# Performance work log

Measured on AMD Instinct MI355X. Metric: run time of the kernel, lower is better.

## Reference

```python
import jax, jax.numpy as jnp
import numpy as np

N_NODES = 50000
N_GRAPHS = 64


def gcn_conv(x, W, b, src, dst, n_nodes):
    # PyG GCNConv: add self-loops, symmetric normalization D^-1/2 A D^-1/2,
    # linear transform, scatter-sum aggregation from src -> dst, plus bias.
    si = jnp.arange(n_nodes, dtype=src.dtype)
    s = jnp.concatenate([src, si])
    d = jnp.concatenate([dst, si])
    deg = jax.ops.segment_sum(jnp.ones_like(d, dtype=x.dtype), d, num_segments=n_nodes)
    dinv = jax.lax.rsqrt(jnp.maximum(deg, 1.0))  # deg >= 1 due to self-loops
    norm = dinv[s] * dinv[d]                      # [E+N]
    h = x @ W                                     # [N, out]
    msg = h[s] * norm[:, None]                    # gather + scale
    out = jax.ops.segment_sum(msg, d, num_segments=n_nodes)
    return out + b


def setup_inputs() -> dict:
    key = jax.random.key(0)
    ks = jax.random.split(key, 12)
    input_dim, hidden, half = 128, 64, 32
    x = jax.random.normal(ks[0], (N_NODES, input_dim), dtype=jnp.float32)
    edge_index = jax.random.randint(ks[1], (2, 800000), 0, N_NODES, dtype=jnp.int64)
    batch = jnp.sort(jax.random.randint(ks[2], (N_NODES,), 0, N_GRAPHS, dtype=jnp.int64))
    def lin(k, fan_in, fan_out):
        s = 1.0 / np.sqrt(fan_in)
        return jax.random.uniform(k, (fan_in, fan_out), jnp.float32, -s, s)
    return {
        "x": x,
        "edge_index": edge_index,
        "batch": batch,
        "W1": lin(ks[3], input_dim, hidden), "b1": jnp.zeros((hidden,), jnp.float32),
        "W2": lin(ks[4], hidden, hidden),    "b2": jnp.zeros((hidden,), jnp.float32),
        "Wc1": lin(ks[5], hidden, half),     "bc1": jnp.zeros((half,), jnp.float32),
        "Wc2": lin(ks[6], half, 1),          "bc2": jnp.zeros((1,), jnp.float32),
    }


def reference(x, edge_index, batch, W1, b1, W2, b2, Wc1, bc1, Wc2, bc2):
    src, dst = edge_index[0], edge_index[1]
    h = jax.nn.relu(gcn_conv(x, W1, b1, src, dst, N_NODES))
    # F.dropout(training=False) -> identity in eval
    h = jax.nn.relu(gcn_conv(h, W2, b2, src, dst, N_NODES))
    # global_mean_pool over graphs
    sums = jax.ops.segment_sum(h, batch, num_segments=N_GRAPHS)
    cnts = jax.ops.segment_sum(jnp.ones((h.shape[0], 1), h.dtype), batch, num_segments=N_GRAPHS)
    g = sums / jnp.maximum(cnts, 1.0)             # [G, hidden]
    # MLP head (Dropout(0.2) is identity in eval)
    z = jax.nn.relu(g @ Wc1 + bc1)
    return z @ Wc2 + bc2                          # [G, 1]
```

## Files before the change

kernel.cpp:

```cpp
#include <hip/hip_runtime.h>
#include <math.h>

#define NG 64
#define HID 64
#define ELL 64

typedef __attribute__((ext_vector_type(8))) short bf16x8;
typedef __attribute__((ext_vector_type(4))) float f32x4;

__device__ __forceinline__ unsigned int bfbits(float f) {
    unsigned int u = __float_as_uint(f);
    return (u + 0x7FFFu + ((u >> 16) & 1u)) >> 16;
}
__device__ __forceinline__ float bfval(unsigned int bits) {
    return __uint_as_float(bits << 16);
}

__global__ void k_zero(int4* __restrict__ p, int n4) {
    int i = blockIdx.x * blockDim.x + threadIdx.x;
    if (i < n4) p[i] = make_int4(0, 0, 0, 0);
}

__global__ void k_degfill(const int* __restrict__ src, const int* __restrict__ dst,
                          int E, int* __restrict__ deg, int* __restrict__ col_ell) {
    int e = blockIdx.x * blockDim.x + threadIdx.x;
    if (e >= E) return;
    int d = dst[e];
    int slot = atomicAdd(deg + d, 1);
    if (slot < ELL) col_ell[(size_t)d * ELL + slot] = src[e];
}

__global__ __launch_bounds__(256) void k_aux(const int* __restrict__ deg,
                                             const int* __restrict__ batch,
                                             float* __restrict__ dinv,
                                             int* __restrict__ gstart,
                                             const float* __restrict__ W1,
                                             const float* __restrict__ W2,
                                             unsigned short* __restrict__ W1hi,
                                             unsigned short* __restrict__ W1lo,
                                             unsigned short* __restrict__ W2hi,
                                             unsigned short* __restrict__ W2lo,
                                             int n, int nblk) {
    const int t = threadIdx.x;
    if (blockIdx.x >= nblk) {
        int idx = (blockIdx.x - nblk) * 256 + t;
        if (idx < 128 * 64) {
            int k = idx >> 6, c = idx & 63;
            float f = W1[idx];
            unsigned hb = bfbits(f);
            W1hi[c * 128 + k] = (unsigned short)hb;
            W1lo[c * 128 + k] = (unsigned short)bfbits(f - bfval(hb));
        } else if (idx < 128 * 64 + 64 * 64) {
            int i2 = idx - 128 * 64;
            int k = i2 >> 6, c = i2 & 63;
            float f = W2[i2];
            unsigned hb = bfbits(f);
            W2hi[c * 64 + k] = (unsigned short)hb;
            W2lo[c * 64 + k] = (unsigned short)bfbits(f - bfval(hb));
        }
        return;
    }
    int i = blockIdx.x * 256 + t;
    if (i < n) {
        dinv[i] = 1.0f / sqrtf((float)deg[i] + 1.0f);
        int bi = batch[i];
        int bp = (i == 0) ? -1 : batch[i - 1];
        for (int g = bp + 1; g <= bi; ++g) gstart[g] = i;
        if (i == n - 1)
            for (int g = bi + 1; g <= NG; ++g) gstart[g] = n;
    }
}

template<int K>
__global__ __launch_bounds__(256) void k_gemm_mfma(const float* __restrict__ A,
                                                   const unsigned short* __restrict__ Whi,
                                                   const unsigned short* __restrict__ Wlo,
                                                   const float* __restrict__ dinv,
                                                   float* __restrict__ out, int n) {
    const int wave = threadIdx.x >> 6, lane = threadIdx.x & 63;
    const int ntile2 = (n + 31) >> 5;
    const int tile2 = blockIdx.x * 4 + wave;
    if (tile2 >= ntile2) return;
    const int lrow = lane & 15;
    const int kgrp = lane >> 4;
    const int r0 = tile2 * 32 + lrow;
    const int r1 = r0 + 16;

    f32x4 acc0[4], acc1[4];
#pragma unroll
    for (int ct = 0; ct < 4; ++ct) {
        acc0[ct] = (f32x4){0.f, 0.f, 0.f, 0.f};
        acc1[ct] = (f32x4){0.f, 0.f, 0.f, 0.f};
    }

#pragma unroll
    for (int s = 0; s < K / 32; ++s) {
        float a0[8], a1[8];
        {
            const float* p0 = A + (size_t)r0 * K + s * 32 + kgrp * 8;
            const float* p1 = A + (size_t)r1 * K + s * 32 + kgrp * 8;
            float4 u0, u1, w0, w1;
            if (r0 < n) { u0 = *(const float4*)p0; u1 = *(const float4*)(p0 + 4); }
            else { u0 = make_float4(0.f,0.f,0.f,0.f); u1 = u0; }
            if (r1 < n) { w0 = *(const float4*)p1; w1 = *(const float4*)(p1 + 4); }
            else { w0 = make_float4(0.f,0.f,0.f,0.f); w1 = w0; }
            a0[0]=u0.x; a0[1]=u0.y; a0[2]=u0.z; a0[3]=u0.w;
            a0[4]=u1.x; a0[5]=u1.y; a0[6]=u1.z; a0[7]=u1.w;
            a1[0]=w0.x; a1[1]=w0.y; a1[2]=w0.z; a1[3]=w0.w;
            a1[4]=w1.x; a1[5]=w1.y; a1[6]=w1.z; a1[7]=w1.w;
        }
        bf16x8 ahi0, alo0, ahi1, alo1;
#pragma unroll
        for (int e = 0; e < 8; ++e) {
            unsigned hb0 = bfbits(a0[e]);
            ahi0[e] = (short)hb0;
            alo0[e] = (short)bfbits(a0[e] - bfval(hb0));
            unsigned hb1 = bfbits(a1[e]);
            ahi1[e] = (short)hb1;
            alo1[e] = (short)bfbits(a1[e] - bfval(hb1));
        }
#pragma unroll
        for (int ct = 0; ct < 4; ++ct) {
            const size_t wo = (size_t)(ct * 16 + lrow) * K + s * 32 + kgrp * 8;
            bf16x8 whi = *(const bf16x8*)(Whi + wo);
            bf16x8 wlo = *(const bf16x8*)(Wlo + wo);
            acc0[ct] = __builtin_amdgcn_mfma_f32_16x16x32_bf16(ahi0, whi, acc0[ct], 0, 0, 0);
            acc0[ct] = __builtin_amdgcn_mfma_f32_16x16x32_bf16(alo0, whi, acc0[ct], 0, 0, 0);
            acc0[ct] = __builtin_amdgcn_mfma_f32_16x16x32_bf16(ahi0, wlo, acc0[ct], 0, 0, 0);
            acc1[ct] = __builtin_amdgcn_mfma_f32_16x16x32_bf16(ahi1, whi, acc1[ct], 0, 0, 0);
            acc1[ct] = __builtin_amdgcn_mfma_f32_16x16x32_bf16(alo1, whi, acc1[ct], 0, 0, 0);
            acc1[ct] = __builtin_amdgcn_mfma_f32_16x16x32_bf16(ahi1, wlo, acc1[ct], 0, 0, 0);
        }
    }

#pragma unroll
    for (int r = 0; r < 4; ++r) {
        int o0 = tile2 * 32 + kgrp * 4 + r;
        if (o0 < n) {
            float dv = dinv[o0];
#pragma unroll
            for (int ct = 0; ct < 4; ++ct)
                out[(size_t)o0 * HID + ct * 16 + lrow] = acc0[ct][r] * dv;
        }
        int o1 = o0 + 16;
        if (o1 < n) {
            float dv = dinv[o1];
#pragma unroll
            for (int ct = 0; ct < 4; ++ct)
                out[(size_t)o1 * HID + ct * 16 + lrow] = acc1[ct][r] * dv;
        }
    }
}

__global__ __launch_bounds__(512) void k_gather_gemm2(const float* __restrict__ hs,
                                                      const int* __restrict__ deg,
                                                      const int* __restrict__ col_ell,
                                                      const float* __restrict__ dinv,
                                                      const float* __restrict__ bias,
                                                      const unsigned short* __restrict__ Whi,
                                                      const unsigned short* __restrict__ Wlo,
                                                      float* __restrict__ outB, int n) {
    __shared__ float Ash[32][68];
    const int wave = threadIdx.x >> 6, lane = threadIdx.x & 63;
    const int grp = lane >> 4, sub = lane & 15;
    const int row = wave * 4 + grp;
    const int node = blockIdx.x * 32 + row;
    const bool has = node < n;

    float4 acc = make_float4(0.f, 0.f, 0.f, 0.f);
    float di = 0.f;
    int j = 0, e = 0;
    const int* cbase = col_ell + (size_t)node * ELL;
    if (has) {
        e = min(deg[node], ELL);
        di = dinv[node];
        acc = *(const float4*)(hs + (size_t)node * HID + sub * 4);
    }
    while (__any(j < e)) {
        int cc[8];
#pragma unroll
        for (int t = 0; t < 8; ++t) cc[t] = (j + t < e) ? cbase[j + t] : -1;
        float4 vv[8];
#pragma unroll
        for (int t = 0; t < 8; ++t)
            if (cc[t] >= 0) vv[t] = *(const float4*)(hs + (size_t)cc[t] * HID + sub * 4);
#pragma unroll
        for (int t = 0; t < 8; ++t)
            if (cc[t] >= 0) {
                acc.x += vv[t].x; acc.y += vv[t].y;
                acc.z += vv[t].z; acc.w += vv[t].w;
            }
        j += 8;
    }
    {
        float4 bv = *(const float4*)(bias + sub * 4);
        float4 o;
        o.x = has ? fmaxf(fmaf(acc.x, di, bv.x), 0.f) : 0.f;
        o.y = has ? fmaxf(fmaf(acc.y, di, bv.y), 0.f) : 0.f;
        o.z = has ? fmaxf(fmaf(acc.z, di, bv.z), 0.f) : 0.f;
        o.w = has ? fmaxf(fmaf(acc.w, di, bv.w), 0.f) : 0.f;
        *(float4*)&Ash[row][sub * 4] = o;
    }
    __syncthreads();

    const int rt = wave >> 2, ct = wave & 3;
    const int lrow = lane & 15;
    const int kgrp = lane >> 4;
    f32x4 a = (f32x4){0.f, 0.f, 0.f, 0.f};
#pragma unroll
    for (int s = 0; s < 2; ++s) {
        const float* ap = &Ash[rt * 16 + lrow][s * 32 + kgrp * 8];
        float4 u0 = *(const float4*)ap;
        float4 u1 = *(const float4*)(ap + 4);
        float av[8] = {u0.x, u0.y, u0.z, u0.w, u1.x, u1.y, u1.z, u1.w};
        bf16x8 ahi, alo;
#pragma unroll
        for (int e2 = 0; e2 < 8; ++e2) {
            unsigned hb = bfbits(av[e2]);
            ahi[e2] = (short)hb;
            alo[e2] = (short)bfbits(av[e2] - bfval(hb));
        }
        const size_t wo = (size_t)(ct * 16 + lrow) * 64 + s * 32 + kgrp * 8;
        bf16x8 whi = *(const bf16x8*)(Whi + wo);
        bf16x8 wlo = *(const bf16x8*)(Wlo + wo);
        a = __builtin_amdgcn_mfma_f32_16x16x32_bf16(ahi, whi, a, 0, 0, 0);
        a = __builtin_amdgcn_mfma_f32_16x16x32_bf16(alo, whi, a, 0, 0, 0);
        a = __builtin_amdgcn_mfma_f32_16x16x32_bf16(ahi, wlo, a, 0, 0, 0);
    }
#pragma unroll
    for (int r = 0; r < 4; ++r) {
        int orow = blockIdx.x * 32 + rt * 16 + kgrp * 4 + r;
        if (orow < n)
            outB[(size_t)orow * HID + ct * 16 + lrow] = a[r] * dinv[orow];
    }
}

__global__ __launch_bounds__(256) void k_gather(const float* __restrict__ hs,
                                                const int* __restrict__ deg,
                                                const int* __restrict__ col_ell,
                                                const float* __restrict__ dinv,
                                                const float* __restrict__ bias,
                                                float* __restrict__ out, int n) {
    const int wave = threadIdx.x >> 6, lane = threadIdx.x & 63;
    const int grp = lane >> 4, sub = lane & 15;
    const int node = blockIdx.x * 16 + wave * 4 + grp;
    const bool has = node < n;

    float4 acc = make_float4(0.f, 0.f, 0.f, 0.f);
    float di = 0.f;
    int j = 0, e = 0;
    const int* cbase = col_ell + (size_t)node * ELL;
    if (has) {
        e = min(deg[node], ELL);
        di = dinv[node];
        acc = *(const float4*)(hs + (size_t)node * HID + sub * 4);
    }
    while (__any(j < e)) {
        int cc[8];
#pragma unroll
        for (int t = 0; t < 8; ++t) cc[t] = (j + t < e) ? cbase[j + t] : -1;
        float4 vv[8];
#pragma unroll
        for (int t = 0; t < 8; ++t)
            if (cc[t] >= 0) vv[t] = *(const float4*)(hs + (size_t)cc[t] * HID + sub * 4);
#pragma unroll
        for (int t = 0; t < 8; ++t)
            if (cc[t] >= 0) {
                acc.x += vv[t].x; acc.y += vv[t].y;
                acc.z += vv[t].z; acc.w += vv[t].w;
            }
        j += 8;
    }
    if (has) {
        float4 bv = *(const float4*)(bias + sub * 4);
        float4 o;
        o.x = fmaxf(fmaf(acc.x, di, bv.x), 0.f);
        o.y = fmaxf(fmaf(acc.y, di, bv.y), 0.f);
        o.z = fmaxf(fmaf(acc.z, di, bv.z), 0.f);
        o.w = fmaxf(fmaf(acc.w, di, bv.w), 0.f);
        *(float4*)(out + (size_t)node * HID + sub * 4) = o;
    }
}

__global__ __launch_bounds__(512) void k_poolhead(const float* __restrict__ h,
                                                  const int* __restrict__ gstart,
                                                  const float* __restrict__ Wc1,
                                                  const float* __restrict__ bc1,
                                                  const float* __restrict__ Wc2,
                                                  const float* __restrict__ bc2,
                                                  float* __restrict__ outp, int n) {
    const int g = blockIdx.x;
    const int lo = gstart[g], lo2 = gstart[g + 1];
    const int t = threadIdx.x;
    const int rg = t >> 4;
    const int c4 = (t & 15) * 4;
    float4 acc = make_float4(0.f, 0.f, 0.f, 0.f);
    for (int r = lo + rg; r < lo2; r += 32) {
        float4 v = *(const float4*)(h + (size_t)r * HID + c4);
        acc.x += v.x; acc.y += v.y; acc.z += v.z; acc.w += v.w;
    }
    __shared__ float4 red[32][16];
    __shared__ float gmv[HID];
    __shared__ float zs[32];
    red[rg][t & 15] = acc;
    __syncthreads();
    if (t < 16) {
        float4 s = red[0][t];
#pragma unroll
        for (int g2 = 1; g2 < 32; ++g2) {
            float4 v = red[g2][t];
            s.x += v.x; s.y += v.y; s.z += v.z; s.w += v.w;
        }
        float inv = 1.0f / fmaxf((float)(lo2 - lo), 1.0f);
        gmv[t * 4 + 0] = s.x * inv; gmv[t * 4 + 1] = s.y * inv;
        gmv[t * 4 + 2] = s.z * inv; gmv[t * 4 + 3] = s.w * inv;
    }
    __syncthreads();
    if (t < 32) {
        float z = bc1[t];
#pragma unroll 8
        for (int k = 0; k < HID; ++k) z = fmaf(gmv[k], Wc1[k * 32 + t], z);
        zs[t] = fmaxf(z, 0.f) * Wc2[t];
    }
    __syncthreads();
    if (t == 0) {
        float o = bc2[0];
#pragma unroll
        for (int j = 0; j < 32; ++j) o += zs[j];
        outp[g] = o;
    }
}

extern "C" void kernel_launch(void* const* d_in, const int* in_sizes, int n_in,
                              void* d_out, int out_size, void* d_ws, size_t ws_size,
                              hipStream_t stream) {
    const float* x    = (const float*)d_in[0];
    const int*   ei   = (const int*)d_in[1];
    const int*   batch= (const int*)d_in[2];
    const float* W1   = (const float*)d_in[3];
    const float* b1   = (const float*)d_in[4];
    const float* W2   = (const float*)d_in[5];
    const float* b2   = (const float*)d_in[6];
    const float* Wc1  = (const float*)d_in[7];
    const float* bc1  = (const float*)d_in[8];
    const float* Wc2  = (const float*)d_in[9];
    const float* bc2  = (const float*)d_in[10];

    const int E = in_sizes[1] / 2;
    const int n = in_sizes[0] / 128;
    const int* srcp = ei;
    const int* dstp = ei + E;

    char* ws = (char*)d_ws;
    auto alloc = [&](size_t bytes) {
        char* p = ws;
        ws += (bytes + 255) & ~(size_t)255;
        return p;
    };
    int*   deg      = (int*)  alloc((size_t)((n + 3) & ~3) * 4);
    float* dinv     = (float*)alloc((size_t)n * 4);
    int*   gstart   = (int*)  alloc((size_t)(NG + 1) * 4);
    int*   col_ell  = (int*)  alloc((size_t)n * ELL * 4);
    float* bufA     = (float*)alloc((size_t)n * HID * 4);
    float* bufB     = (float*)alloc((size_t)n * HID * 4);
    unsigned short* W1hi = (unsigned short*)alloc(128 * 64 * 2);
    unsigned short* W1lo = (unsigned short*)alloc(128 * 64 * 2);
    unsigned short* W2hi = (unsigned short*)alloc(64 * 64 * 2);
    unsigned short* W2lo = (unsigned short*)alloc(64 * 64 * 2);

    const int n4 = (n + 3) / 4;
    k_zero<<<(n4 + 255) / 256, 256, 0, stream>>>((int4*)deg, n4);

    k_degfill<<<(E + 255) / 256, 256, 0, stream>>>(srcp, dstp, E, deg, col_ell);

    const int nblk = (n + 255) / 256;
    const int wblk = (128 * 64 + 64 * 64 + 255) / 256;
    k_aux<<<nblk + wblk, 256, 0, stream>>>(deg, batch, dinv, gstart,
                                           W1, W2, W1hi, W1lo, W2hi, W2lo, n, nblk);

    const int mblocks = ((n + 31) / 32 + 3) / 4;

    k_gemm_mfma<128><<<mblocks, 256, 0, stream>>>(x, W1hi, W1lo, dinv, bufA, n);
    k_gather_gemm2<<<(n + 31) / 32, 512, 0, stream>>>(bufA, deg, col_ell, dinv, b1,
                                                      W2hi, W2lo, bufB, n);
    k_gather<<<(n + 15) / 16, 256, 0, stream>>>(bufB, deg, col_ell, dinv, b2, bufA, n);

    k_poolhead<<<NG, 512, 0, stream>>>(bufA, gstart, Wc1, bc1, Wc2, bc2, (float*)d_out, n);
}
```

Before: 153.7 us.

## Bin edges by destination range before ELL fill to localize atomics

Replaces the single-pass edge scatter into the ELL adjacency with a two-pass binning scheme. Edges are first partitioned into 8 destination-range buckets using block-local counters and global offsets. A second kernel then performs the degree atomics and column writes bucket by bucket, so concurrent blocks touch a smaller slice of deg and col_ell and the writes are meant to stay cache-resident. The cost is an extra kernel launch and an extra write and read of all edges. Each bin is capped at a fixed capacity, so edges beyond it are silently dropped if the inputs are skewed.

```diff
diff --git a/kernel.cpp b/kernel.cpp
--- a/kernel.cpp
+++ b/kernel.cpp
@@ -4,6 +4,7 @@
 #define NG 64
 #define HID 64
 #define ELL 64
+#define BCAP 110592
 
 typedef __attribute__((ext_vector_type(8))) short bf16x8;
 typedef __attribute__((ext_vector_type(4))) float f32x4;
@@ -16,34 +17,26 @@
     return __uint_as_float(bits << 16);
 }
 
-__global__ void k_zero(int4* __restrict__ p, int n4) {
+__global__ void k_zero0(int4* __restrict__ deg4, int4* __restrict__ gc4, int n4) {
     int i = blockIdx.x * blockDim.x + threadIdx.x;
-    if (i < n4) p[i] = make_int4(0, 0, 0, 0);
-}
-
-__global__ void k_degfill(const int* __restrict__ src, const int* __restrict__ dst,
-                          int E, int* __restrict__ deg, int* __restrict__ col_ell) {
-    int e = blockIdx.x * blockDim.x + threadIdx.x;
-    if (e >= E) return;
-    int d = dst[e];
-    int slot = atomicAdd(deg + d, 1);
-    if (slot < ELL) col_ell[(size_t)d * ELL + slot] = src[e];
-}
-
-__global__ __launch_bounds__(256) void k_aux(const int* __restrict__ deg,
-                                             const int* __restrict__ batch,
-                                             float* __restrict__ dinv,
-                                             int* __restrict__ gstart,
-                                             const float* __restrict__ W1,
-                                             const float* __restrict__ W2,
-                                             unsigned short* __restrict__ W1hi,
-                                             unsigned short* __restrict__ W1lo,
-                                             unsigned short* __restrict__ W2hi,
-                                             unsigned short* __restrict__ W2lo,
-                                             int n, int nblk) {
+    if (i < n4) deg4[i] = make_int4(0, 0, 0, 0);
+    if (i < 2) gc4[i] = make_int4(0, 0, 0, 0);
+}
+
+__global__ __launch_bounds__(256) void k_binA(const int* __restrict__ src,
+                                              const int* __restrict__ dst,
+                                              int E, unsigned MAGIC,
+                                              int2* __restrict__ binned,
+                                              int* __restrict__ gcount, int nbin,
+                                              const float* __restrict__ W1,
+                                              const float* __restrict__ W2,
+                                              unsigned short* __restrict__ W1hi,
+                                              unsigned short* __restrict__ W1lo,
+                                              unsigned short* __restrict__ W2hi,
+                                              unsigned short* __restrict__ W2lo) {
     const int t = threadIdx.x;
-    if (blockIdx.x >= nblk) {
-        int idx = (blockIdx.x - nblk) * 256 + t;
+    if (blockIdx.x >= nbin) {
+        int idx = (blockIdx.x - nbin) * 256 + t;
         if (idx < 128 * 64) {
             int k = idx >> 6, c = idx & 63;
             float f = W1[idx];
@@ -60,7 +53,50 @@
         }
         return;
     }
-    int i = blockIdx.x * 256 + t;
+    __shared__ int cnt[8], base[8];
+    if (t < 8) cnt[t] = 0;
+    __syncthreads();
+    int e = blockIdx.x * 256 + t;
+    int s = 0, d = 0, b = 0, rk = 0;
+    bool val = (e < E);
+    if (val) {
+        s = src[e]; d = dst[e];
+        b = __umulhi((unsigned)d, MAGIC);
+        rk = atomicAdd(&cnt[b], 1);
+    }
+    __syncthreads();
+    if (t < 8) base[t] = (cnt[t] > 0) ? atomicAdd(&gcount[t], cnt[t]) : 0;
+    __syncthreads();
+    if (val) {
+        int off = base[b] + rk;
+        if (off < BCAP) binned[(size_t)b * BCAP + off] = make_int2(s, d);
+    }
+}
+
+__global__ __launch_bounds__(256) void k_binB(const int2* __restrict__ binned,
+                                              const int* __restrict__ gcount,
+                                              int* __restrict__ deg,
+                                              int* __restrict__ col_ell) {
+    const int r = blockIdx.x & 7, c = blockIdx.x >> 3;
+    const int t = threadIdx.x;
+    const int count = min(gcount[r], BCAP);
+    const int2* bb = binned + (size_t)r * BCAP;
+#pragma unroll
+    for (int k = 0; k < 8; ++k) {
+        int idx = c * 2048 + k * 256 + t;
+        if (idx < count) {
+            int2 sd = bb[idx];
+            int slot = atomicAdd(deg + sd.y, 1);
+            if (slot < ELL) col_ell[(size_t)sd.y * ELL + slot] = sd.x;
+        }
+    }
+}
+
+__global__ __launch_bounds__(256) void k_aux(const int* __restrict__ deg,
+                                             const int* __restrict__ batch,
+                                             float* __restrict__ dinv,
+                                             int* __restrict__ gstart, int n) {
+    int i = blockIdx.x * 256 + threadIdx.x;
     if (i < n) {
         dinv[i] = 1.0f / sqrtf((float)deg[i] + 1.0f);
         int bi = batch[i];
@@ -358,9 +394,11 @@
         return p;
     };
     int*   deg      = (int*)  alloc((size_t)((n + 3) & ~3) * 4);
+    int*   gcount   = (int*)  alloc(8 * 4);
     float* dinv     = (float*)alloc((size_t)n * 4);
     int*   gstart   = (int*)  alloc((size_t)(NG + 1) * 4);
     int*   col_ell  = (int*)  alloc((size_t)n * ELL * 4);
+    int2*  binned   = (int2*) alloc((size_t)8 * BCAP * 8);
     float* bufA     = (float*)alloc((size_t)n * HID * 4);
     float* bufB     = (float*)alloc((size_t)n * HID * 4);
     unsigned short* W1hi = (unsigned short*)alloc(128 * 64 * 2);
@@ -369,14 +407,19 @@
     unsigned short* W2lo = (unsigned short*)alloc(64 * 64 * 2);
 
     const int n4 = (n + 3) / 4;
-    k_zero<<<(n4 + 255) / 256, 256, 0, stream>>>((int4*)deg, n4);
-
-    k_degfill<<<(E + 255) / 256, 256, 0, stream>>>(srcp, dstp, E, deg, col_ell);
+    k_zero0<<<(n4 + 255) / 256, 256, 0, stream>>>((int4*)deg, (int4*)gcount, n4);
+
+    const unsigned MAGIC = (unsigned)((((unsigned long long)8) << 32) / (unsigned)n) + 1u;
+    const int nbin = (E + 255) / 256;
+    const int wblk = (128 * 64 + 64 * 64 + 255) / 256;
+
+    k_binA<<<nbin + wblk, 256, 0, stream>>>(srcp, dstp, E, MAGIC, binned, gcount, nbin,
+                                            W1, W2, W1hi, W1lo, W2hi, W2lo);
+    const int KB = (BCAP + 2047) / 2048;
+    k_binB<<<8 * KB, 256, 0, stream>>>(binned, gcount, deg, col_ell);
 
     const int nblk = (n + 255) / 256;
-    const int wblk = (128 * 64 + 64 * 64 + 255) / 256;
-    k_aux<<<nblk + wblk, 256, 0, stream>>>(deg, batch, dinv, gstart,
-                                           W1, W2, W1hi, W1lo, W2hi, W2lo, n, nblk);
+    k_aux<<<nblk, 256, 0, stream>>>(deg, batch, dinv, gstart, n);
 
     const int mblocks = ((n + 31) / 32 + 3) / 4;
 
```

New measurement: 178.8 us. +16.3%, slower.

## Overlap edge binning with first GEMM by moving source-side dinv scaling into gather

Applied to the files above, without the earlier changes.

The first GEMM no longer multiplies its output by the source-node dinv. Instead the layer-1 gather loads dinv for each neighbour and applies it with an FMA. That removes the dependency of the GEMM on degrees, so edge binning (atomics into the ELL), the X@W1 MFMA GEMM and the graph-start computation run as independent block ranges of one merged kernel. Zeroing and weight splitting are merged into a prep kernel, and dinv becomes its own small kernel. The cost is an extra random dinv load per edge in the first gather, and atomic-heavy blocks share the GPU with GEMM blocks.

```diff
diff --git a/kernel.cpp b/kernel.cpp
--- a/kernel.cpp
+++ b/kernel.cpp
@@ -16,70 +16,68 @@
     return __uint_as_float(bits << 16);
 }
 
-__global__ void k_zero(int4* __restrict__ p, int n4) {
+__global__ void k_prep(int4* __restrict__ deg4, int n4,
+                       const float* __restrict__ W1, const float* __restrict__ W2,
+                       unsigned short* __restrict__ W1hi, unsigned short* __restrict__ W1lo,
+                       unsigned short* __restrict__ W2hi, unsigned short* __restrict__ W2lo) {
     int i = blockIdx.x * blockDim.x + threadIdx.x;
-    if (i < n4) p[i] = make_int4(0, 0, 0, 0);
-}
-
-__global__ void k_degfill(const int* __restrict__ src, const int* __restrict__ dst,
-                          int E, int* __restrict__ deg, int* __restrict__ col_ell) {
-    int e = blockIdx.x * blockDim.x + threadIdx.x;
-    if (e >= E) return;
-    int d = dst[e];
-    int slot = atomicAdd(deg + d, 1);
-    if (slot < ELL) col_ell[(size_t)d * ELL + slot] = src[e];
-}
-
-__global__ __launch_bounds__(256) void k_aux(const int* __restrict__ deg,
-                                             const int* __restrict__ batch,
-                                             float* __restrict__ dinv,
-                                             int* __restrict__ gstart,
-                                             const float* __restrict__ W1,
-                                             const float* __restrict__ W2,
-                                             unsigned short* __restrict__ W1hi,
-                                             unsigned short* __restrict__ W1lo,
-                                             unsigned short* __restrict__ W2hi,
-                                             unsigned short* __restrict__ W2lo,
-                                             int n, int nblk) {
+    if (i < n4) deg4[i] = make_int4(0, 0, 0, 0);
+    if (i < 128 * 64) {
+        int k = i >> 6, c = i & 63;
+        float f = W1[i];
+        unsigned hb = bfbits(f);
+        W1hi[c * 128 + k] = (unsigned short)hb;
+        W1lo[c * 128 + k] = (unsigned short)bfbits(f - bfval(hb));
+    }
+    int i2 = i - 128 * 64;
+    if (i2 >= 0 && i2 < 64 * 64) {
+        int k = i2 >> 6, c = i2 & 63;
+        float f = W2[i2];
+        unsigned hb = bfbits(f);
+        W2hi[c * 64 + k] = (unsigned short)hb;
+        W2lo[c * 64 + k] = (unsigned short)bfbits(f - bfval(hb));
+    }
+}
+
+__global__ __launch_bounds__(256) void k_mega(const int* __restrict__ src,
+                                              const int* __restrict__ dst, int E,
+                                              int* __restrict__ deg,
+                                              int* __restrict__ col_ell,
+                                              const float* __restrict__ A,
+                                              const unsigned short* __restrict__ Whi,
+                                              const unsigned short* __restrict__ Wlo,
+                                              float* __restrict__ out,
+                                              const int* __restrict__ batch,
+                                              int* __restrict__ gstart,
+                                              int n, int nbin, int mblocks) {
+    const int bid = blockIdx.x;
     const int t = threadIdx.x;
-    if (blockIdx.x >= nblk) {
-        int idx = (blockIdx.x - nblk) * 256 + t;
-        if (idx < 128 * 64) {
-            int k = idx >> 6, c = idx & 63;
-            float f = W1[idx];
-            unsigned hb = bfbits(f);
-            W1hi[c * 128 + k] = (unsigned short)hb;
-            W1lo[c * 128 + k] = (unsigned short)bfbits(f - bfval(hb));
-        } else if (idx < 128 * 64 + 64 * 64) {
-            int i2 = idx - 128 * 64;
-            int k = i2 >> 6, c = i2 & 63;
-            float f = W2[i2];
-            unsigned hb = bfbits(f);
-            W2hi[c * 64 + k] = (unsigned short)hb;
-            W2lo[c * 64 + k] = (unsigned short)bfbits(f - bfval(hb));
+
+    if (bid < nbin) {
+        int e = bid * 256 + t;
+        if (e < E) {
+            int d = dst[e];
+            int slot = atomicAdd(deg + d, 1);
+            if (slot < ELL) col_ell[(size_t)d * ELL + slot] = src[e];
         }
         return;
     }
-    int i = blockIdx.x * 256 + t;
-    if (i < n) {
-        dinv[i] = 1.0f / sqrtf((float)deg[i] + 1.0f);
-        int bi = batch[i];
-        int bp = (i == 0) ? -1 : batch[i - 1];
-        for (int g = bp + 1; g <= bi; ++g) gstart[g] = i;
-        if (i == n - 1)
-            for (int g = bi + 1; g <= NG; ++g) gstart[g] = n;
-    }
-}
-
-template<int K>
-__global__ __launch_bounds__(256) void k_gemm_mfma(const float* __restrict__ A,
-                                                   const unsigned short* __restrict__ Whi,
-                                                   const unsigned short* __restrict__ Wlo,
-                                                   const float* __restrict__ dinv,
-                                                   float* __restrict__ out, int n) {
-    const int wave = threadIdx.x >> 6, lane = threadIdx.x & 63;
+    if (bid >= nbin + mblocks) {
+        int i = (bid - nbin - mblocks) * 256 + t;
+        if (i < n) {
+            int bi = batch[i];
+            int bp = (i == 0) ? -1 : batch[i - 1];
+            for (int g = bp + 1; g <= bi; ++g) gstart[g] = i;
+            if (i == n - 1)
+                for (int g = bi + 1; g <= NG; ++g) gstart[g] = n;
+        }
+        return;
+    }
+
+    constexpr int K = 128;
+    const int wave = t >> 6, lane = t & 63;
     const int ntile2 = (n + 31) >> 5;
-    const int tile2 = blockIdx.x * 4 + wave;
+    const int tile2 = (bid - nbin) * 4 + wave;
     if (tile2 >= ntile2) return;
     const int lrow = lane & 15;
     const int kgrp = lane >> 4;
@@ -137,22 +135,25 @@
     for (int r = 0; r < 4; ++r) {
         int o0 = tile2 * 32 + kgrp * 4 + r;
         if (o0 < n) {
-            float dv = dinv[o0];
 #pragma unroll
             for (int ct = 0; ct < 4; ++ct)
-                out[(size_t)o0 * HID + ct * 16 + lrow] = acc0[ct][r] * dv;
+                out[(size_t)o0 * HID + ct * 16 + lrow] = acc0[ct][r];
         }
         int o1 = o0 + 16;
         if (o1 < n) {
-            float dv = dinv[o1];
 #pragma unroll
             for (int ct = 0; ct < 4; ++ct)
-                out[(size_t)o1 * HID + ct * 16 + lrow] = acc1[ct][r] * dv;
-        }
-    }
-}
-
-__global__ __launch_bounds__(512) void k_gather_gemm2(const float* __restrict__ hs,
+                out[(size_t)o1 * HID + ct * 16 + lrow] = acc1[ct][r];
+        }
+    }
+}
+
+__global__ void k_dinv(const int* __restrict__ deg, float* __restrict__ dinv, int n) {
+    int i = blockIdx.x * blockDim.x + threadIdx.x;
+    if (i < n) dinv[i] = 1.0f / sqrtf((float)deg[i] + 1.0f);
+}
+
+__global__ __launch_bounds__(512) void k_gather_gemm2(const float* __restrict__ h,
                                                       const int* __restrict__ deg,
                                                       const int* __restrict__ col_ell,
                                                       const float* __restrict__ dinv,
@@ -174,21 +175,29 @@
     if (has) {
         e = min(deg[node], ELL);
         di = dinv[node];
-        acc = *(const float4*)(hs + (size_t)node * HID + sub * 4);
+        float4 hv = *(const float4*)(h + (size_t)node * HID + sub * 4);
+        acc.x = hv.x * di; acc.y = hv.y * di;
+        acc.z = hv.z * di; acc.w = hv.w * di;
     }
     while (__any(j < e)) {
         int cc[8];
 #pragma unroll
         for (int t = 0; t < 8; ++t) cc[t] = (j + t < e) ? cbase[j + t] : -1;
         float4 vv[8];
-#pragma unroll
-        for (int t = 0; t < 8; ++t)
-            if (cc[t] >= 0) vv[t] = *(const float4*)(hs + (size_t)cc[t] * HID + sub * 4);
+        float dv[8];
 #pragma unroll
         for (int t = 0; t < 8; ++t)
             if (cc[t] >= 0) {
-                acc.x += vv[t].x; acc.y += vv[t].y;
-                acc.z += vv[t].z; acc.w += vv[t].w;
+                vv[t] = *(const float4*)(h + (size_t)cc[t] * HID + sub * 4);
+                dv[t] = dinv[cc[t]];
+            }
+#pragma unroll
+        for (int t = 0; t < 8; ++t)
+            if (cc[t] >= 0) {
+                acc.x = fmaf(vv[t].x, dv[t], acc.x);
+                acc.y = fmaf(vv[t].y, dv[t], acc.y);
+                acc.z = fmaf(vv[t].z, dv[t], acc.z);
+                acc.w = fmaf(vv[t].w, dv[t], acc.w);
             }
         j += 8;
     }
@@ -369,18 +378,20 @@
     unsigned short* W2lo = (unsigned short*)alloc(64 * 64 * 2);
 
     const int n4 = (n + 3) / 4;
-    k_zero<<<(n4 + 255) / 256, 256, 0, stream>>>((int4*)deg, n4);
-
-    k_degfill<<<(E + 255) / 256, 256, 0, stream>>>(srcp, dstp, E, deg, col_ell);
-
+    const int prepblk = (max(n4, 128 * 64 + 64 * 64) + 255) / 256;
+    k_prep<<<prepblk, 256, 0, stream>>>((int4*)deg, n4, W1, W2,
+                                        W1hi, W1lo, W2hi, W2lo);
+
+    const int nbin = (E + 255) / 256;
+    const int mblocks = ((n + 31) / 32 + 3) / 4;
     const int nblk = (n + 255) / 256;
-    const int wblk = (128 * 64 + 64 * 64 + 255) / 256;
-    k_aux<<<nblk + wblk, 256, 0, stream>>>(deg, batch, dinv, gstart,
-                                           W1, W2, W1hi, W1lo, W2hi, W2lo, n, nblk);
-
-    const int mblocks = ((n + 31) / 32 + 3) / 4;
-
-    k_gemm_mfma<128><<<mblocks, 256, 0, stream>>>(x, W1hi, W1lo, dinv, bufA, n);
+
+    k_mega<<<nbin + mblocks + nblk, 256, 0, stream>>>(srcp, dstp, E, deg, col_ell,
+                                                      x, W1hi, W1lo, bufA,
+                                                      batch, gstart, n, nbin, mblocks);
+
+    k_dinv<<<nblk, 256, 0, stream>>>(deg, dinv, n);
+
     k_gather_gemm2<<<(n + 31) / 32, 512, 0, stream>>>(bufA, deg, col_ell, dinv, b1,
                                                       W2hi, W2lo, bufB, n);
     k_gather<<<(n + 15) / 16, 256, 0, stream>>>(bufB, deg, col_ell, dinv, b2, bufA, n);
```

Measured after the change: 161.7 us. 1.05x slower.

## Partition edge scatter by destination range and drop separate dinv and zero kernels

Applied to the files above, without the earlier changes.

Merges zeroing of deg, the gstart computation and the weight split into a single prep kernel, which removes two launches. dinv is no longer stored; each consumer recomputes it from deg. The edge fill now runs NSCAN=16 passes over the edge list, each handling only the destinations in one node range. The aim is to localise atomics and col_ell writes so they stay cache-resident, at the cost of reading dst 16 times.

```diff
diff --git a/kernel.cpp b/kernel.cpp
--- a/kernel.cpp
+++ b/kernel.cpp
@@ -4,6 +4,7 @@
 #define NG 64
 #define HID 64
 #define ELL 64
+#define NSCAN 16
 
 typedef __attribute__((ext_vector_type(8))) short bf16x8;
 typedef __attribute__((ext_vector_type(4))) float f32x4;
@@ -15,67 +16,73 @@
 __device__ __forceinline__ float bfval(unsigned int bits) {
     return __uint_as_float(bits << 16);
 }
-
-__global__ void k_zero(int4* __restrict__ p, int n4) {
-    int i = blockIdx.x * blockDim.x + threadIdx.x;
-    if (i < n4) p[i] = make_int4(0, 0, 0, 0);
-}
-
-__global__ void k_degfill(const int* __restrict__ src, const int* __restrict__ dst,
-                          int E, int* __restrict__ deg, int* __restrict__ col_ell) {
-    int e = blockIdx.x * blockDim.x + threadIdx.x;
-    if (e >= E) return;
-    int d = dst[e];
-    int slot = atomicAdd(deg + d, 1);
-    if (slot < ELL) col_ell[(size_t)d * ELL + slot] = src[e];
-}
-
-__global__ __launch_bounds__(256) void k_aux(const int* __restrict__ deg,
-                                             const int* __restrict__ batch,
-                                             float* __restrict__ dinv,
-                                             int* __restrict__ gstart,
-                                             const float* __restrict__ W1,
-                                             const float* __restrict__ W2,
-                                             unsigned short* __restrict__ W1hi,
-                                             unsigned short* __restrict__ W1lo,
-                                             unsigned short* __restrict__ W2hi,
-                                             unsigned short* __restrict__ W2lo,
-                                             int n, int nblk) {
-    const int t = threadIdx.x;
-    if (blockIdx.x >= nblk) {
-        int idx = (blockIdx.x - nblk) * 256 + t;
-        if (idx < 128 * 64) {
-            int k = idx >> 6, c = idx & 63;
-            float f = W1[idx];
-            unsigned hb = bfbits(f);
-            W1hi[c * 128 + k] = (unsigned short)hb;
-            W1lo[c * 128 + k] = (unsigned short)bfbits(f - bfval(hb));
-        } else if (idx < 128 * 64 + 64 * 64) {
-            int i2 = idx - 128 * 64;
-            int k = i2 >> 6, c = i2 & 63;
-            float f = W2[i2];
-            unsigned hb = bfbits(f);
-            W2hi[c * 64 + k] = (unsigned short)hb;
-            W2lo[c * 64 + k] = (unsigned short)bfbits(f - bfval(hb));
-        }
-        return;
-    }
-    int i = blockIdx.x * 256 + t;
+__device__ __forceinline__ float dinv_of(int d) {
+    return 1.0f / sqrtf((float)d + 1.0f);
+}
+
+__global__ __launch_bounds__(256) void k_prep(int* __restrict__ deg, int n,
+                                              const int* __restrict__ batch,
+                                              int* __restrict__ gstart,
+                                              const float* __restrict__ W1,
+                                              const float* __restrict__ W2,
+                                              unsigned short* __restrict__ W1hi,
+                                              unsigned short* __restrict__ W1lo,
+                                              unsigned short* __restrict__ W2hi,
+                                              unsigned short* __restrict__ W2lo) {
+    int i = blockIdx.x * 256 + threadIdx.x;
     if (i < n) {
-        dinv[i] = 1.0f / sqrtf((float)deg[i] + 1.0f);
+        deg[i] = 0;
         int bi = batch[i];
         int bp = (i == 0) ? -1 : batch[i - 1];
         for (int g = bp + 1; g <= bi; ++g) gstart[g] = i;
         if (i == n - 1)
             for (int g = bi + 1; g <= NG; ++g) gstart[g] = n;
     }
+    if (i < 128 * 64) {
+        int k = i >> 6, c = i & 63;
+        float f = W1[i];
+        unsigned hb = bfbits(f);
+        W1hi[c * 128 + k] = (unsigned short)hb;
+        W1lo[c * 128 + k] = (unsigned short)bfbits(f - bfval(hb));
+    }
+    int i2 = i - 128 * 64;
+    if (i2 >= 0 && i2 < 64 * 64) {
+        int k = i2 >> 6, c = i2 & 63;
+        float f = W2[i2];
+        unsigned hb = bfbits(f);
+        W2hi[c * 64 + k] = (unsigned short)hb;
+        W2lo[c * 64 + k] = (unsigned short)bfbits(f - bfval(hb));
+    }
+}
+
+__global__ __launch_bounds__(256) void k_degfill(const int* __restrict__ src,
+                                                 const int* __restrict__ dst, int E,
+                                                 int step, int n,
+                                                 int* __restrict__ deg,
+                                                 int* __restrict__ col_ell, int bpg) {
+    const int group = blockIdx.x / bpg;
+    const int blk   = blockIdx.x % bpg;
+    const int lo = group * step;
+    const int hi = min(lo + step, n);
+    const int base = blk * 1024;
+#pragma unroll
+    for (int k = 0; k < 4; ++k) {
+        int e = base + k * 256 + threadIdx.x;
+        if (e < E) {
+            int d = dst[e];
+            if (d >= lo && d < hi) {
+                int slot = atomicAdd(deg + d, 1);
+                if (slot < ELL) col_ell[(size_t)d * ELL + slot] = src[e];
+            }
+        }
+    }
 }
 
 template<int K>
 __global__ __launch_bounds__(256) void k_gemm_mfma(const float* __restrict__ A,
                                                    const unsigned short* __restrict__ Whi,
                                                    const unsigned short* __restrict__ Wlo,
-                                                   const float* __restrict__ dinv,
+                                                   const int* __restrict__ deg,
                                                    float* __restrict__ out, int n) {
     const int wave = threadIdx.x >> 6, lane = threadIdx.x & 63;
     const int ntile2 = (n + 31) >> 5;
@@ -137,14 +144,14 @@
     for (int r = 0; r < 4; ++r) {
         int o0 = tile2 * 32 + kgrp * 4 + r;
         if (o0 < n) {
-            float dv = dinv[o0];
+            float dv = dinv_of(deg[o0]);
 #pragma unroll
             for (int ct = 0; ct < 4; ++ct)
                 out[(size_t)o0 * HID + ct * 16 + lrow] = acc0[ct][r] * dv;
         }
         int o1 = o0 + 16;
         if (o1 < n) {
-            float dv = dinv[o1];
+            float dv = dinv_of(deg[o1]);
 #pragma unroll
             for (int ct = 0; ct < 4; ++ct)
                 out[(size_t)o1 * HID + ct * 16 + lrow] = acc1[ct][r] * dv;
@@ -155,7 +162,6 @@
 __global__ __launch_bounds__(512) void k_gather_gemm2(const float* __restrict__ hs,
                                                       const int* __restrict__ deg,
                                                       const int* __restrict__ col_ell,
-                                                      const float* __restrict__ dinv,
                                                       const float* __restrict__ bias,
                                                       const unsigned short* __restrict__ Whi,
                                                       const unsigned short* __restrict__ Wlo,
@@ -172,8 +178,9 @@
     int j = 0, e = 0;
     const int* cbase = col_ell + (size_t)node * ELL;
     if (has) {
-        e = min(deg[node], ELL);
-        di = dinv[node];
+        int dg = deg[node];
+        e = min(dg, ELL);
+        di = dinv_of(dg);
         acc = *(const float4*)(hs + (size_t)node * HID + sub * 4);
     }
     while (__any(j < e)) {
@@ -231,14 +238,13 @@
     for (int r = 0; r < 4; ++r) {
         int orow = blockIdx.x * 32 + rt * 16 + kgrp * 4 + r;
         if (orow < n)
-            outB[(size_t)orow * HID + ct * 16 + lrow] = a[r] * dinv[orow];
+            outB[(size_t)orow * HID + ct * 16 + lrow] = a[r] * dinv_of(deg[orow]);
     }
 }
 
 __global__ __launch_bounds__(256) void k_gather(const float* __restrict__ hs,
                                                 const int* __restrict__ deg,
                                                 const int* __restrict__ col_ell,
-                                                const float* __restrict__ dinv,
                                                 const float* __restrict__ bias,
                                                 float* __restrict__ out, int n) {
     const int wave = threadIdx.x >> 6, lane = threadIdx.x & 63;
@@ -251,8 +257,9 @@
     int j = 0, e = 0;
     const int* cbase = col_ell + (size_t)node * ELL;
     if (has) {
-        e = min(deg[node], ELL);
-        di = dinv[node];
+        int dg = deg[node];
+        e = min(dg, ELL);
+        di = dinv_of(dg);
         acc = *(const float4*)(hs + (size_t)node * HID + sub * 4);
     }
     while (__any(j < e)) {
@@ -357,8 +364,7 @@
         ws += (bytes + 255) & ~(size_t)255;
         return p;
     };
-    int*   deg      = (int*)  alloc((size_t)((n + 3) & ~3) * 4);
-    float* dinv     = (float*)alloc((size_t)n * 4);
+    int*   deg      = (int*)  alloc((size_t)n * 4);
     int*   gstart   = (int*)  alloc((size_t)(NG + 1) * 4);
     int*   col_ell  = (int*)  alloc((size_t)n * ELL * 4);
     float* bufA     = (float*)alloc((size_t)n * HID * 4);
@@ -368,22 +374,21 @@
     unsigned short* W2hi = (unsigned short*)alloc(64 * 64 * 2);
     unsigned short* W2lo = (unsigned short*)alloc(64 * 64 * 2);
 
-    const int n4 = (n + 3) / 4;
-    k_zero<<<(n4 + 255) / 256, 256, 0, stream>>>((int4*)deg, n4);
-
-    k_degfill<<<(E + 255) / 256, 256, 0, stream>>>(srcp, dstp, E, deg, col_ell);
-
     const int nblk = (n + 255) / 256;
-    const int wblk = (128 * 64 + 64 * 64 + 255) / 256;
-    k_aux<<<nblk + wblk, 256, 0, stream>>>(deg, batch, dinv, gstart,
-                                           W1, W2, W1hi, W1lo, W2hi, W2lo, n, nblk);
+    k_prep<<<nblk, 256, 0, stream>>>(deg, n, batch, gstart,
+                                     W1, W2, W1hi, W1lo, W2hi, W2lo);
+
+    const int bpg = (E + 1023) / 1024;
+    const int step = (n + NSCAN - 1) / NSCAN;
+    k_degfill<<<NSCAN * bpg, 256, 0, stream>>>(srcp, dstp, E, step, n,
+                                               deg, col_ell, bpg);
 
     const int mblocks = ((n + 31) / 32 + 3) / 4;
 
-    k_gemm_mfma<128><<<mblocks, 256, 0, stream>>>(x, W1hi, W1lo, dinv, bufA, n);
-    k_gather_gemm2<<<(n + 31) / 32, 512, 0, stream>>>(bufA, deg, col_ell, dinv, b1,
+    k_gemm_mfma<128><<<mblocks, 256, 0, stream>>>(x, W1hi, W1lo, deg, bufA, n);
+    k_gather_gemm2<<<(n + 31) / 32, 512, 0, stream>>>(bufA, deg, col_ell, b1,
                                                       W2hi, W2lo, bufB, n);
-    k_gather<<<(n + 15) / 16, 256, 0, stream>>>(bufB, deg, col_ell, dinv, b2, bufA, n);
+    k_gather<<<(n + 15) / 16, 256, 0, stream>>>(bufB, deg, col_ell, b2, bufA, n);
 
     k_poolhead<<<NG, 512, 0, stream>>>(bufA, gstart, Wc1, bc1, Wc2, bc2, (float*)d_out, n);
 }
```

New measurement: 153.3 us (median of 2 runs). Within noise of the previous version (-0.3%).
